# Kernel optimization log

Measured on AMD Instinct MI355X. Metric: run time of the kernel, lower is better.

The kernel has to match this reference:

```python
import jax, jax.numpy as jnp
import numpy as np

N_WIRES = 8
DIM = 1 << N_WIRES  # 256

# --- static precompute: CNOT-ring basis permutation and PauliZ sign matrix ---
# torchquantum convention: wire 0 is the most significant bit of the basis index.
_gates = [(w, w + 1) for w in range(N_WIRES - 1)] + [(N_WIRES - 1, 0)]
_perm = np.empty(DIM, dtype=np.int64)
for b in range(DIM):
    bits = [(b >> (N_WIRES - 1 - w)) & 1 for w in range(N_WIRES)]
    for c, t in _gates:
        if bits[c]:
            bits[t] ^= 1
    _perm[b] = sum(bit << (N_WIRES - 1 - w) for w, bit in enumerate(bits))
_Z = np.array([[1.0 - 2.0 * ((idx >> (N_WIRES - 1 - w)) & 1) for w in range(N_WIRES)]
               for idx in range(DIM)], dtype=np.float32)
# exp_Z[w] = sum_b probs_in[b] * Z[perm[b], w]  (CNOTs permute basis states)
_M = jnp.asarray(_Z[_perm])  # [256, 8]


def _quantum_head(angles):
    """angles: [..., 8] RX angles -> PauliZ expectations [..., 8].

    Circuit: RX(angle_w) on each wire from |0>, CNOT ring, MeasureAll(PauliZ).
    Post-RX state is a product state; CNOTs only permute basis states, so
    probabilities suffice (no complex amplitudes needed).
    """
    half = angles * 0.5
    c2 = jnp.cos(half) ** 2  # P(qubit=0)
    s2 = jnp.sin(half) ** 2  # P(qubit=1)
    # Build the 256-dim joint probability vector via sequential outer products.
    p = jnp.ones(angles.shape[:-1] + (1,), angles.dtype)
    for w in range(N_WIRES):
        pw = jnp.stack([c2[..., w], s2[..., w]], axis=-1)  # [..., 2]
        p = (p[..., :, None] * pw[..., None, :]).reshape(angles.shape[:-1] + (-1,))
    return p @ _M.astype(p.dtype)  # [..., 8]


def setup_inputs() -> dict:
    key = jax.random.key(0)
    ks = jax.random.split(key, 6)
    B, S, E = 8, 512, 768
    scale = 1.0 / np.sqrt(E)
    return {
        "x": jax.random.normal(ks[0], (B, S, E), jnp.float32),
        "W_proj": jax.random.normal(ks[1], (E, E), jnp.float32) * scale,
        "b_proj": jax.random.normal(ks[2], (E,), jnp.float32) * 0.02,
        "theta": jax.random.normal(ks[3], (N_WIRES,), jnp.float32),
        "W_comb": jax.random.normal(ks[4], (E, E), jnp.float32) * scale,
        "b_comb": jax.random.normal(ks[5], (E,), jnp.float32) * 0.02,
    }


def reference(x, W_proj, b_proj, theta, W_comb, b_comb):
    B, S, E = x.shape
    H = E // N_WIRES  # num_heads = 96
    proj = x @ W_proj.T + b_proj                 # [B, S, E] (torch Linear)
    angles = proj.reshape(B, S, H, N_WIRES) + theta  # encoder RX(x) then RX(theta): angles add
    expz = _quantum_head(angles)                 # [B, S, H, 8]
    out = expz.reshape(B, S, E)                  # heads re-concatenated
    # dropout is identity in eval mode
    return out @ W_comb.T + b_comb
```

## Files before the change

kernel.cpp:

```cpp
#include <hip/hip_runtime.h>

typedef _Float16 v8h __attribute__((ext_vector_type(8)));
typedef float    v4f __attribute__((ext_vector_type(4)));

__device__ __forceinline__ void gl_lds16(const void* g, void* l) {
  __builtin_amdgcn_global_load_lds(
      (__attribute__((address_space(1))) void*)(void*)g,
      (__attribute__((address_space(3))) void*)l, 16, 0, 0);
}

__global__ void conv_w(const float4* __restrict__ wp, const float4* __restrict__ wc,
                       v8h* __restrict__ op, v8h* __restrict__ oc) {
  const int n = 73728;
  int i = blockIdx.x * blockDim.x + threadIdx.x;
  const float4* src = (i < n) ? wp : wc;
  v8h* dst = (i < n) ? op : oc;
  const int j = (i < n) ? i : i - n;
  const float4 a = src[2 * j];
  const float4 b = src[2 * j + 1];
  v8h o;
  o[0] = (_Float16)a.x; o[1] = (_Float16)a.y; o[2] = (_Float16)a.z; o[3] = (_Float16)a.w;
  o[4] = (_Float16)b.x; o[5] = (_Float16)b.y; o[6] = (_Float16)b.z; o[7] = (_Float16)b.w;
  dst[j] = o;
}


__global__ __launch_bounds__(256) void gemm1_qh(
    const float* __restrict__ X,
    const _Float16* __restrict__ B,
    const float* __restrict__ bp,
    const float* __restrict__ theta,
    _Float16* __restrict__ EZ) {
  const int t = threadIdx.x;
  const int b = blockIdx.x;
  const int xcd = b & 7, slot = b >> 3;
  const int bm = xcd * 8 + slot / 12;
  const int bn = slot % 12;

  const int wave = t >> 6, lane = t & 63;
  const int quad = lane >> 4, l16 = lane & 15;
  const int wm = (wave >> 1) * 32, wn = (wave & 1) * 32;

  __shared__ __align__(16) unsigned char smem[32768];
  _Float16* As = (_Float16*)smem;
  _Float16* Bs = (_Float16*)(smem + 16384);
  float* Cs = (float*)smem;

  const float4 th0 = *(const float4*)theta;
  const float4 th1 = *(const float4*)(theta + 4);

  const int tr = t >> 4;
  const int tc = t & 15;
  const int cgl = tc ^ tr;

  const float*    Xg = X + (size_t)(bm * 64 + tr) * 768 + cgl * 8;
  const _Float16* Bg = B + (size_t)(bn * 64 + tr) * 768 + cgl * 8;

  v4f acc[2][2];
#pragma unroll
  for (int i = 0; i < 2; i++)
#pragma unroll
    for (int j = 0; j < 2; j++) acc[i][j] = (v4f){0.f, 0.f, 0.f, 0.f};

  for (int kt = 0; kt < 768; kt += 128) {
#pragma unroll
    for (int c = 0; c < 4; c++)
      gl_lds16(Bg + (size_t)c * 16 * 768 + kt, &Bs[c * 2048 + t * 8]);
#pragma unroll
    for (int c = 0; c < 4; c++) {
      const float* p = Xg + (size_t)c * 16 * 768 + kt;
      const float4 a0 = *(const float4*)p;
      const float4 a1 = *(const float4*)(p + 4);
      v8h av;
      av[0] = (_Float16)a0.x; av[1] = (_Float16)a0.y; av[2] = (_Float16)a0.z; av[3] = (_Float16)a0.w;
      av[4] = (_Float16)a1.x; av[5] = (_Float16)a1.y; av[6] = (_Float16)a1.z; av[7] = (_Float16)a1.w;
      *(v8h*)&As[c * 2048 + t * 8] = av;
    }
    __syncthreads();
#pragma unroll
    for (int q = 0; q < 4; q++) {
      v8h af[2], bf[2];
#pragma unroll
      for (int i = 0; i < 2; i++)
        af[i] = *(const v8h*)&As[(wm + i * 16 + l16) * 128 + (((q * 4 + quad) ^ l16) * 8)];
#pragma unroll
      for (int j = 0; j < 2; j++)
        bf[j] = *(const v8h*)&Bs[(wn + j * 16 + l16) * 128 + (((q * 4 + quad) ^ l16) * 8)];
#pragma unroll
      for (int i = 0; i < 2; i++)
#pragma unroll
        for (int j = 0; j < 2; j++)
          acc[i][j] = __builtin_amdgcn_mfma_f32_16x16x32_f16(af[i], bf[j], acc[i][j], 0, 0, 0);
    }
    __syncthreads();
  }

  const int r0 = wm + quad * 4;
  const int c0 = wn + l16;
#pragma unroll
  for (int j = 0; j < 2; j++)
#pragma unroll
    for (int i = 0; i < 2; i++)
#pragma unroll
      for (int r = 0; r < 4; r++)
        Cs[(r0 + i * 16 + r) * 68 + c0 + j * 16] = acc[i][j][r];
  __syncthreads();

#pragma unroll
  for (int s = 0; s < 2; s++) {
    const int idx = t + s * 256;
    const int row = idx >> 3, h = idx & 7;
    const int gcol = bn * 64 + h * 8;
    const float* cr = &Cs[row * 68 + h * 8];
    const float4 q0 = *(const float4*)cr;
    const float4 q1 = *(const float4*)(cr + 4);
    const float4 b0 = *(const float4*)(bp + gcol);
    const float4 b1 = *(const float4*)(bp + gcol + 4);
    float c[8];
    c[0] = cosf(q0.x + b0.x + th0.x);
    c[1] = cosf(q0.y + b0.y + th0.y);
    c[2] = cosf(q0.z + b0.z + th0.z);
    c[3] = cosf(q0.w + b0.w + th0.w);
    c[4] = cosf(q1.x + b1.x + th1.x);
    c[5] = cosf(q1.y + b1.y + th1.y);
    c[6] = cosf(q1.z + b1.z + th1.z);
    c[7] = cosf(q1.w + b1.w + th1.w);
    float e[8];
    e[0] = c[1] * c[2] * c[3] * c[4] * c[5] * c[6] * c[7];
    float pr = c[0];
#pragma unroll
    for (int w = 1; w < 8; w++) { pr *= c[w]; e[w] = pr; }
    v8h ov;
#pragma unroll
    for (int w = 0; w < 8; w++) ov[w] = (_Float16)e[w];
    *(v8h*)(EZ + (size_t)(bm * 64 + row) * 768 + gcol) = ov;
  }
}

__global__ __launch_bounds__(256) void gemm2(
    const _Float16* __restrict__ A,
    const _Float16* __restrict__ B,
    float* __restrict__ C,
    const float* __restrict__ bias) {
  const int t = threadIdx.x;
  const int b = blockIdx.x;
  const int xcd = b & 7, slot = b >> 3;
  const int bm = xcd * 8 + slot / 12;
  const int bn = slot % 12;

  const int wave = t >> 6, lane = t & 63;
  const int quad = lane >> 4, l16 = lane & 15;
  const int wm = (wave >> 1) * 32, wn = (wave & 1) * 32;

  __shared__ __align__(16) _Float16 As[64 * 128];
  __shared__ __align__(16) _Float16 Bs[64 * 128];

  const int tr = t >> 4;
  const int tc = t & 15;
  const int cgl = tc ^ tr;

  const _Float16* Ag = A + (size_t)(bm * 64 + tr) * 768 + cgl * 8;
  const _Float16* Bg = B + (size_t)(bn * 64 + tr) * 768 + cgl * 8;

  v4f acc[2][2];
#pragma unroll
  for (int i = 0; i < 2; i++)
#pragma unroll
    for (int j = 0; j < 2; j++) acc[i][j] = (v4f){0.f, 0.f, 0.f, 0.f};

  for (int kt = 0; kt < 768; kt += 128) {
#pragma unroll
    for (int c = 0; c < 4; c++) {
      gl_lds16(Ag + (size_t)c * 16 * 768 + kt, &As[c * 2048 + t * 8]);
      gl_lds16(Bg + (size_t)c * 16 * 768 + kt, &Bs[c * 2048 + t * 8]);
    }
    __syncthreads();
#pragma unroll
    for (int q = 0; q < 4; q++) {
      v8h af[2], bf[2];
#pragma unroll
      for (int i = 0; i < 2; i++)
        af[i] = *(const v8h*)&As[(wm + i * 16 + l16) * 128 + (((q * 4 + quad) ^ l16) * 8)];
#pragma unroll
      for (int j = 0; j < 2; j++)
        bf[j] = *(const v8h*)&Bs[(wn + j * 16 + l16) * 128 + (((q * 4 + quad) ^ l16) * 8)];
#pragma unroll
      for (int i = 0; i < 2; i++)
#pragma unroll
        for (int j = 0; j < 2; j++)
          acc[i][j] = __builtin_amdgcn_mfma_f32_16x16x32_f16(af[i], bf[j], acc[i][j], 0, 0, 0);
    }
    __syncthreads();
  }

  const int row0 = bm * 64 + wm + quad * 4;
  const int col0 = bn * 64 + wn + l16;
#pragma unroll
  for (int j = 0; j < 2; j++) {
    const int col = col0 + j * 16;
    const float bv = bias[col];
#pragma unroll
    for (int i = 0; i < 2; i++) {
#pragma unroll
      for (int r = 0; r < 4; r++) {
        C[(size_t)(row0 + i * 16 + r) * 768 + col] = acc[i][j][r] + bv;
      }
    }
  }
}

extern "C" void kernel_launch(void* const* d_in, const int* in_sizes, int n_in,
                              void* d_out, int out_size, void* d_ws, size_t ws_size,
                              hipStream_t stream) {
  const float* x     = (const float*)d_in[0];
  const float* Wp    = (const float*)d_in[1];
  const float* bp    = (const float*)d_in[2];
  const float* theta = (const float*)d_in[3];
  const float* Wcf   = (const float*)d_in[4];
  const float* bc    = (const float*)d_in[5];
  float* out = (float*)d_out;

  const int M = 4096, E = 768;
  const size_t ME = (size_t)M * E;
  const size_t EE = (size_t)E * E;

  _Float16* WPH = (_Float16*)d_ws;
  _Float16* WCH = WPH + EE;
  _Float16* EZ  = WCH + EE;

  conv_w<<<(int)(2 * EE / 8 / 256), 256, 0, stream>>>(
      (const float4*)Wp, (const float4*)Wcf, (v8h*)WPH, (v8h*)WCH);

  gemm1_qh<<<768, 256, 0, stream>>>(x, WPH, bp, theta, EZ);

  gemm2<<<768, 256, 0, stream>>>(EZ, WCH, out, bc);
}
```

Baseline: 99.28 us.

## Double-buffer LDS tiles with K=64 stages and register-prefetch X in both GEMMs

Both GEMM kernels now use a two-stage LDS ping-pong with a K-tile of 64 instead of single-buffered 128-wide tiles. The next tile's global-to-LDS loads are issued before computing the current one, and gemm1 also prefetches X two stages ahead into registers. This overlaps memory latency with MFMA work and removes one barrier per iteration. The cost is more loop iterations, more registers for the prefetched X, and a changed XOR swizzle that has to stay consistent between the store and read paths.

```diff
diff --git a/kernel.cpp b/kernel.cpp
--- a/kernel.cpp
+++ b/kernel.cpp
@@ -7,6 +7,12 @@
   __builtin_amdgcn_global_load_lds(
       (__attribute__((address_space(1))) void*)(void*)g,
       (__attribute__((address_space(3))) void*)l, 16, 0, 0);
+}
+__device__ __forceinline__ v8h cvt8(const float4 a, const float4 b) {
+  v8h o;
+  o[0] = (_Float16)a.x; o[1] = (_Float16)a.y; o[2] = (_Float16)a.z; o[3] = (_Float16)a.w;
+  o[4] = (_Float16)b.x; o[5] = (_Float16)b.y; o[6] = (_Float16)b.z; o[7] = (_Float16)b.w;
+  return o;
 }
 
 __global__ void conv_w(const float4* __restrict__ wp, const float4* __restrict__ wc,
@@ -16,12 +22,7 @@
   const float4* src = (i < n) ? wp : wc;
   v8h* dst = (i < n) ? op : oc;
   const int j = (i < n) ? i : i - n;
-  const float4 a = src[2 * j];
-  const float4 b = src[2 * j + 1];
-  v8h o;
-  o[0] = (_Float16)a.x; o[1] = (_Float16)a.y; o[2] = (_Float16)a.z; o[3] = (_Float16)a.w;
-  o[4] = (_Float16)b.x; o[5] = (_Float16)b.y; o[6] = (_Float16)b.z; o[7] = (_Float16)b.w;
-  dst[j] = o;
+  dst[j] = cvt8(src[2 * j], src[2 * j + 1]);
 }
 
 
@@ -49,12 +50,10 @@
   const float4 th0 = *(const float4*)theta;
   const float4 th1 = *(const float4*)(theta + 4);
 
-  const int tr = t >> 4;
-  const int tc = t & 15;
-  const int cgl = tc ^ tr;
-
-  const float*    Xg = X + (size_t)(bm * 64 + tr) * 768 + cgl * 8;
-  const _Float16* Bg = B + (size_t)(bn * 64 + tr) * 768 + cgl * 8;
+  const int row_s = t >> 3;
+  const int cgl_s = (t & 7) ^ (row_s & 7);
+  const float*    Xg = X + (size_t)(bm * 64 + row_s) * 768 + cgl_s * 8;
+  const _Float16* Bg = B + (size_t)(bn * 64 + row_s) * 768 + cgl_s * 8;
 
   v4f acc[2][2];
 #pragma unroll
@@ -62,39 +61,59 @@
 #pragma unroll
     for (int j = 0; j < 2; j++) acc[i][j] = (v4f){0.f, 0.f, 0.f, 0.f};
 
-  for (int kt = 0; kt < 768; kt += 128) {
-#pragma unroll
-    for (int c = 0; c < 4; c++)
-      gl_lds16(Bg + (size_t)c * 16 * 768 + kt, &Bs[c * 2048 + t * 8]);
-#pragma unroll
-    for (int c = 0; c < 4; c++) {
-      const float* p = Xg + (size_t)c * 16 * 768 + kt;
-      const float4 a0 = *(const float4*)p;
-      const float4 a1 = *(const float4*)(p + 4);
-      v8h av;
-      av[0] = (_Float16)a0.x; av[1] = (_Float16)a0.y; av[2] = (_Float16)a0.z; av[3] = (_Float16)a0.w;
-      av[4] = (_Float16)a1.x; av[5] = (_Float16)a1.y; av[6] = (_Float16)a1.z; av[7] = (_Float16)a1.w;
-      *(v8h*)&As[c * 2048 + t * 8] = av;
-    }
+#pragma unroll
+  for (int c = 0; c < 2; c++) {
+    const float* p = Xg + (size_t)c * 32 * 768;
+    *(v8h*)&As[c * 2048 + t * 8] = cvt8(*(const float4*)p, *(const float4*)(p + 4));
+    gl_lds16(Bg + (size_t)c * 32 * 768, &Bs[c * 2048 + t * 8]);
+  }
+  float4 xr[2][2];
+#pragma unroll
+  for (int c = 0; c < 2; c++) {
+    const float* p = Xg + (size_t)c * 32 * 768 + 64;
+    xr[c][0] = *(const float4*)p;
+    xr[c][1] = *(const float4*)(p + 4);
+  }
+
+  for (int i = 0; i < 12; i++) {
     __syncthreads();
-#pragma unroll
-    for (int q = 0; q < 4; q++) {
+    if (i + 1 < 12) {
+      const int nb = (i + 1) & 1;
+#pragma unroll
+      for (int c = 0; c < 2; c++) {
+        *(v8h*)&As[nb * 4096 + c * 2048 + t * 8] = cvt8(xr[c][0], xr[c][1]);
+        gl_lds16(Bg + (size_t)c * 32 * 768 + (i + 1) * 64, &Bs[nb * 4096 + c * 2048 + t * 8]);
+      }
+    }
+    if (i + 2 < 12) {
+#pragma unroll
+      for (int c = 0; c < 2; c++) {
+        const float* p = Xg + (size_t)c * 32 * 768 + (i + 2) * 64;
+        xr[c][0] = *(const float4*)p;
+        xr[c][1] = *(const float4*)(p + 4);
+      }
+    }
+    const _Float16* as_ = As + (i & 1) * 4096;
+    const _Float16* bs_ = Bs + (i & 1) * 4096;
+#pragma unroll
+    for (int q = 0; q < 2; q++) {
+      const int cg = ((q * 4 + quad) ^ (l16 & 7)) * 8;
       v8h af[2], bf[2];
 #pragma unroll
-      for (int i = 0; i < 2; i++)
-        af[i] = *(const v8h*)&As[(wm + i * 16 + l16) * 128 + (((q * 4 + quad) ^ l16) * 8)];
+      for (int ii = 0; ii < 2; ii++)
+        af[ii] = *(const v8h*)&as_[(wm + ii * 16 + l16) * 64 + cg];
 #pragma unroll
       for (int j = 0; j < 2; j++)
-        bf[j] = *(const v8h*)&Bs[(wn + j * 16 + l16) * 128 + (((q * 4 + quad) ^ l16) * 8)];
-#pragma unroll
-      for (int i = 0; i < 2; i++)
+        bf[j] = *(const v8h*)&bs_[(wn + j * 16 + l16) * 64 + cg];
+#pragma unroll
+      for (int ii = 0; ii < 2; ii++)
 #pragma unroll
         for (int j = 0; j < 2; j++)
-          acc[i][j] = __builtin_amdgcn_mfma_f32_16x16x32_f16(af[i], bf[j], acc[i][j], 0, 0, 0);
-    }
-    __syncthreads();
-  }
-
+          acc[ii][j] = __builtin_amdgcn_mfma_f32_16x16x32_f16(af[ii], bf[j], acc[ii][j], 0, 0, 0);
+    }
+  }
+
+  __syncthreads();
   const int r0 = wm + quad * 4;
   const int c0 = wn + l16;
 #pragma unroll
@@ -152,15 +171,13 @@
   const int quad = lane >> 4, l16 = lane & 15;
   const int wm = (wave >> 1) * 32, wn = (wave & 1) * 32;
 
-  __shared__ __align__(16) _Float16 As[64 * 128];
-  __shared__ __align__(16) _Float16 Bs[64 * 128];
-
-  const int tr = t >> 4;
-  const int tc = t & 15;
-  const int cgl = tc ^ tr;
-
-  const _Float16* Ag = A + (size_t)(bm * 64 + tr) * 768 + cgl * 8;
-  const _Float16* Bg = B + (size_t)(bn * 64 + tr) * 768 + cgl * 8;
+  __shared__ __align__(16) _Float16 As[2][4096];
+  __shared__ __align__(16) _Float16 Bs[2][4096];
+
+  const int row_s = t >> 3;
+  const int cgl_s = (t & 7) ^ (row_s & 7);
+  const _Float16* Ag = A + (size_t)(bm * 64 + row_s) * 768 + cgl_s * 8;
+  const _Float16* Bg = B + (size_t)(bn * 64 + row_s) * 768 + cgl_s * 8;
 
   v4f acc[2][2];
 #pragma unroll
@@ -168,29 +185,41 @@
 #pragma unroll
     for (int j = 0; j < 2; j++) acc[i][j] = (v4f){0.f, 0.f, 0.f, 0.f};
 
-  for (int kt = 0; kt < 768; kt += 128) {
-#pragma unroll
-    for (int c = 0; c < 4; c++) {
-      gl_lds16(Ag + (size_t)c * 16 * 768 + kt, &As[c * 2048 + t * 8]);
-      gl_lds16(Bg + (size_t)c * 16 * 768 + kt, &Bs[c * 2048 + t * 8]);
-    }
+#pragma unroll
+  for (int c = 0; c < 2; c++) {
+    gl_lds16(Ag + (size_t)c * 32 * 768, &As[0][c * 2048 + t * 8]);
+    gl_lds16(Bg + (size_t)c * 32 * 768, &Bs[0][c * 2048 + t * 8]);
+  }
+
+  for (int i = 0; i < 12; i++) {
     __syncthreads();
-#pragma unroll
-    for (int q = 0; q < 4; q++) {
+    if (i + 1 < 12) {
+      const int nb = (i + 1) & 1;
+      const int kt = (i + 1) * 64;
+#pragma unroll
+      for (int c = 0; c < 2; c++) {
+        gl_lds16(Ag + (size_t)c * 32 * 768 + kt, &As[nb][c * 2048 + t * 8]);
+        gl_lds16(Bg + (size_t)c * 32 * 768 + kt, &Bs[nb][c * 2048 + t * 8]);
+      }
+    }
+    const _Float16* as_ = As[i & 1];
+    const _Float16* bs_ = Bs[i & 1];
+#pragma unroll
+    for (int q = 0; q < 2; q++) {
+      const int cg = ((q * 4 + quad) ^ (l16 & 7)) * 8;
       v8h af[2], bf[2];
 #pragma unroll
-      for (int i = 0; i < 2; i++)
-        af[i] = *(const v8h*)&As[(wm + i * 16 + l16) * 128 + (((q * 4 + quad) ^ l16) * 8)];
+      for (int ii = 0; ii < 2; ii++)
+        af[ii] = *(const v8h*)&as_[(wm + ii * 16 + l16) * 64 + cg];
 #pragma unroll
       for (int j = 0; j < 2; j++)
-        bf[j] = *(const v8h*)&Bs[(wn + j * 16 + l16) * 128 + (((q * 4 + quad) ^ l16) * 8)];
-#pragma unroll
-      for (int i = 0; i < 2; i++)
+        bf[j] = *(const v8h*)&bs_[(wn + j * 16 + l16) * 64 + cg];
+#pragma unroll
+      for (int ii = 0; ii < 2; ii++)
 #pragma unroll
         for (int j = 0; j < 2; j++)
-          acc[i][j] = __builtin_amdgcn_mfma_f32_16x16x32_f16(af[i], bf[j], acc[i][j], 0, 0, 0);
-    }
-    __syncthreads();
+          acc[ii][j] = __builtin_amdgcn_mfma_f32_16x16x32_f16(af[ii], bf[j], acc[ii][j], 0, 0, 0);
+    }
   }
 
   const int row0 = bm * 64 + wm + quad * 4;
@@ -220,9 +249,7 @@
   const float* bc    = (const float*)d_in[5];
   float* out = (float*)d_out;
 
-  const int M = 4096, E = 768;
-  const size_t ME = (size_t)M * E;
-  const size_t EE = (size_t)E * E;
+  const size_t EE = (size_t)768 * 768;
 
   _Float16* WPH = (_Float16*)d_ws;
   _Float16* WCH = WPH + EE;
```

Measured after the change: 102.1 us. +2.8%, slower.
